# Kernel tuning notes

Hardware: AMD Instinct MI355X
Metric: run time of the kernel (lower is better)

## Reference

```python
import jax, jax.numpy as jnp
import numpy as np

NUM_HEADS = 16
NEG_INF = -1000000.0  # matches torch masked_fill value


def setup_inputs() -> dict:
    key = jax.random.key(0)
    k1, k2, k3, k4, k5, k6 = jax.random.split(key, 6)
    N, S, E = 2, 2048, 1024
    x_encoder = jax.random.normal(k1, (N, S, E), dtype=jnp.float32)
    x_decoder = jax.random.normal(k2, (N, S, E), dtype=jnp.float32)
    mask = jax.random.randint(k3, (S, S), 0, 2, dtype=jnp.int32)
    W_qk = jax.random.normal(k4, (2 * E, E), dtype=jnp.float32) * (1.0 / np.sqrt(E))
    W_v = jax.random.normal(k5, (E, E), dtype=jnp.float32) * (1.0 / np.sqrt(E))
    W_o = jax.random.normal(k6, (E, E), dtype=jnp.float32) * (1.0 / np.sqrt(E))
    return {"x_encoder": x_encoder, "x_decoder": x_decoder, "mask": mask,
            "W_qk": W_qk, "W_v": W_v, "W_o": W_o}


def reference(x_encoder, x_decoder, mask, W_qk, W_v, W_o):
    N, S, E = x_encoder.shape
    H = NUM_HEADS
    hd = E // H
    # projections (no bias)
    qk = x_encoder @ W_qk.T            # (N, S, 2E)
    v = x_decoder @ W_v.T              # (N, S, E)
    qk = qk.reshape(N, S, H, 2 * hd).transpose(0, 2, 1, 3)  # (N, H, S, 2hd)
    v = v.reshape(N, S, H, hd).transpose(0, 2, 1, 3)         # (N, H, S, hd)
    q, k = qk[..., :hd], qk[..., hd:]
    # scaled dot-product attention with mask fill
    logits = jnp.einsum('bhqd,bhkd->bhqk', q, k) / jnp.sqrt(jnp.float32(hd))
    m = mask[None, None, :, :]  # expand_mask: 2D -> (1,1,S,S)
    logits = jnp.where(m == 0, jnp.float32(NEG_INF), logits)
    attn = jax.nn.softmax(logits, axis=-1)
    vals = jnp.einsum('bhqk,bhkd->bhqd', attn, v)            # (N, H, S, hd)
    vals = vals.transpose(0, 2, 1, 3).reshape(N, S, E)
    return vals @ W_o.T
```

## Files before the change

kernel.cpp:

```cpp
#include <hip/hip_runtime.h>

typedef __attribute__((ext_vector_type(8))) short short8;
typedef __attribute__((ext_vector_type(4))) float f32x4;
typedef __attribute__((ext_vector_type(4))) unsigned short u16x4;
typedef __attribute__((ext_vector_type(4))) unsigned int u32x4;

#define MFMA16(A,B,C) __builtin_amdgcn_mfma_f32_16x16x32_bf16(A,B,C,0,0,0)

__device__ __forceinline__ unsigned short f2bf(float f) {
  unsigned int u = __builtin_bit_cast(unsigned int, f);
  unsigned int r = (u + 0x7fffu + ((u >> 16) & 1u)) >> 16;
  return (unsigned short)r;
}

__device__ __forceinline__ unsigned int cvt_pk_bf16(float lo, float hi) {
  unsigned int r;
  asm("v_cvt_pk_bf16_f32 %0, %1, %2" : "=v"(r) : "v"(lo), "v"(hi));
  return r;
}

__device__ __forceinline__ f32x4 zero4() {
  f32x4 z; z.x = 0.f; z.y = 0.f; z.z = 0.f; z.w = 0.f; return z;
}

__device__ __forceinline__ void gl_lds16(const void* g, void* l) {
  __builtin_amdgcn_global_load_lds((const __attribute__((address_space(1))) void*)g,
                                   (__attribute__((address_space(3))) void*)l, 16, 0, 0);
}

__global__ __launch_bounds__(256) void cvt_all(const float* __restrict__ xe,
                                               const float* __restrict__ xd,
                                               const float* __restrict__ wqk,
                                               const float* __restrict__ wv,
                                               const float* __restrict__ wo,
                                               unsigned short* __restrict__ ws) {
  long i = (long)blockIdx.x * 256 + threadIdx.x;
  const float* src; unsigned short* dst; long o; bool scl = false;
  if (i < 1048576)      { src = xe;  dst = ws + 8650752;  o = i; }
  else if (i < 2097152) { src = xd;  dst = ws + 12845056; o = i - 1048576; }
  else if (i < 2621440) { src = wqk; dst = ws + 17039360; o = i - 2097152;
                          scl = (((o >> 8) & 127) < 64); }
  else if (i < 2883584) { src = wv;  dst = ws + 19136512; o = i - 2621440; }
  else                  { src = wo;  dst = ws + 20185088; o = i - 2883584; }
  float4 f = ((const float4*)src)[o];
  if (scl) {
    const float SCQ = 0.125f * 1.4426950408889634f;
    f.x *= SCQ; f.y *= SCQ; f.z *= SCQ; f.w *= SCQ;
  }
  u16x4 r; r.x = f2bf(f.x); r.y = f2bf(f.y); r.z = f2bf(f.z); r.w = f2bf(f.w);
  ((u16x4*)dst)[o] = r;
}

__global__ __launch_bounds__(256) void mask_pack(const int* __restrict__ mask,
                                                 unsigned int* __restrict__ mbits) {
  int idx = blockIdx.x * 256 + threadIdx.x;
  int row = idx >> 6, wi = idx & 63;
  const int* p = mask + (long)row * 2048 + wi * 32;
  unsigned int bits = 0;
  #pragma unroll
  for (int j = 0; j < 32; j++) bits |= (p[j] != 0 ? 1u : 0u) << j;
  mbits[idx] = bits;
}

template <int MODE>
__global__ __launch_bounds__(256) void gemm_bt(const unsigned short* __restrict__ A,
                                               const unsigned short* __restrict__ B,
                                               void* __restrict__ Cv,
                                               int M, int N, int K) {
  __shared__ __align__(16) unsigned short As[128 * 64];
  __shared__ __align__(16) unsigned short Bs[128 * 64];
  const int tid = threadIdx.x;
  const int w = tid >> 6, l = tid & 63;
  const int wr = w >> 1, wc = w & 1;
  const long row0 = (long)blockIdx.y * 128;
  const long col0 = (long)blockIdx.x * 128;
  const int lr = l >> 3;
  const int lc = (l & 7) * 8;

  f32x4 acc[4][4];
  #pragma unroll
  for (int m = 0; m < 4; m++)
    #pragma unroll
    for (int n = 0; n < 4; n++) acc[m][n] = zero4();

  for (int k0 = 0; k0 < K; k0 += 64) {
    #pragma unroll
    for (int j = 0; j < 4; j++) {
      int slot = j * 4 + w;
      int row = slot * 8 + lr;
      gl_lds16(A + (row0 + row) * K + k0 + lc, &As[slot * 512]);
      gl_lds16(B + (col0 + row) * K + k0 + lc, &Bs[slot * 512]);
    }
    __syncthreads();
    #pragma unroll
    for (int kk = 0; kk < 2; kk++) {
      short8 a[4], b[4];
      #pragma unroll
      for (int m = 0; m < 4; m++)
        a[m] = *(const short8*)&As[(wr * 64 + m * 16 + (l & 15)) * 64 + kk * 32 + (l >> 4) * 8];
      #pragma unroll
      for (int n = 0; n < 4; n++)
        b[n] = *(const short8*)&Bs[(wc * 64 + n * 16 + (l & 15)) * 64 + kk * 32 + (l >> 4) * 8];
      #pragma unroll
      for (int m = 0; m < 4; m++)
        #pragma unroll
        for (int n = 0; n < 4; n++)
          acc[m][n] = MFMA16(a[m], b[n], acc[m][n]);
    }
    __syncthreads();
  }

  #pragma unroll
  for (int m = 0; m < 4; m++) {
    long rowb = row0 + wr * 64 + m * 16 + ((l >> 4) * 4);
    #pragma unroll
    for (int n = 0; n < 4; n++) {
      long colb = col0 + wc * 64 + n * 16 + (l & 15);
      if (MODE == 0) {
        unsigned short* C = (unsigned short*)Cv;
        #pragma unroll
        for (int r = 0; r < 4; r++) C[(rowb + r) * N + colb] = f2bf(acc[m][n][r]);
      } else if (MODE == 1) {
        unsigned short* C = (unsigned short*)Cv;
        long bb = rowb >> 11, s0 = rowb & 2047;
        u16x4 pk;
        pk.x = f2bf(acc[m][n][0]); pk.y = f2bf(acc[m][n][1]);
        pk.z = f2bf(acc[m][n][2]); pk.w = f2bf(acc[m][n][3]);
        *(u16x4*)&C[(bb * 1024 + colb) * 2048 + s0] = pk;
      } else {
        float* C = (float*)Cv;
        #pragma unroll
        for (int r = 0; r < 4; r++) C[(rowb + r) * N + colb] = acc[m][n][r];
      }
    }
  }
}

__device__ __forceinline__ void softmax_pack(const f32x4* sf, unsigned long long mw,
                                             int g, int sA, int sB, int gh,
                                             float& l_run, short8& pa0o, short8& pa1o) {
  mw >>= (g * 4);
  unsigned int mlo = (unsigned int)mw, mhi = (unsigned int)(mw >> 32);
  float pv[16];
  float lsum = 0.f;
  #pragma unroll
  for (int kvq = 0; kvq < 4; kvq++) {
    unsigned int msel = (kvq < 2) ? mlo : mhi;
    #pragma unroll
    for (int r = 0; r < 4; r++) {
      float e = __builtin_amdgcn_exp2f(sf[kvq][r]);
      unsigned int bit = (msel >> (((kvq & 1) << 4) + r)) & 1u;
      float p = bit ? e : 0.0f;
      pv[kvq * 4 + r] = p;
      lsum += p;
    }
  }
  l_run += lsum;

  unsigned int pk0[2], pk1[2], pk2[2], pk3[2];
  pk0[0] = cvt_pk_bf16(pv[0],  pv[1]);  pk0[1] = cvt_pk_bf16(pv[2],  pv[3]);
  pk1[0] = cvt_pk_bf16(pv[4],  pv[5]);  pk1[1] = cvt_pk_bf16(pv[6],  pv[7]);
  pk2[0] = cvt_pk_bf16(pv[8],  pv[9]);  pk2[1] = cvt_pk_bf16(pv[10], pv[11]);
  pk3[0] = cvt_pk_bf16(pv[12], pv[13]); pk3[1] = cvt_pk_bf16(pv[14], pv[15]);

  u32x4 a0, a1;
  int t0, t1;
  t0 = __shfl((int)pk0[0], sA); t1 = __shfl((int)pk1[0], sA);
  a0.x = gh ? (unsigned)t1 : (unsigned)t0;
  t0 = __shfl((int)pk0[1], sA); t1 = __shfl((int)pk1[1], sA);
  a0.y = gh ? (unsigned)t1 : (unsigned)t0;
  t0 = __shfl((int)pk0[0], sB); t1 = __shfl((int)pk1[0], sB);
  a0.z = gh ? (unsigned)t1 : (unsigned)t0;
  t0 = __shfl((int)pk0[1], sB); t1 = __shfl((int)pk1[1], sB);
  a0.w = gh ? (unsigned)t1 : (unsigned)t0;
  t0 = __shfl((int)pk2[0], sA); t1 = __shfl((int)pk3[0], sA);
  a1.x = gh ? (unsigned)t1 : (unsigned)t0;
  t0 = __shfl((int)pk2[1], sA); t1 = __shfl((int)pk3[1], sA);
  a1.y = gh ? (unsigned)t1 : (unsigned)t0;
  t0 = __shfl((int)pk2[0], sB); t1 = __shfl((int)pk3[0], sB);
  a1.z = gh ? (unsigned)t1 : (unsigned)t0;
  t0 = __shfl((int)pk2[1], sB); t1 = __shfl((int)pk3[1], sB);
  a1.w = gh ? (unsigned)t1 : (unsigned)t0;
  pa0o = __builtin_bit_cast(short8, a0);
  pa1o = __builtin_bit_cast(short8, a1);
}

__global__ __launch_bounds__(256, 4) void attn(const unsigned short* __restrict__ qk,
                                               const unsigned short* __restrict__ vT,
                                               const unsigned int* __restrict__ mbits,
                                               unsigned short* __restrict__ po0,
                                               unsigned short* __restrict__ po1,
                                               float* __restrict__ pl0,
                                               float* __restrict__ pl1) {
  __shared__ __align__(16) unsigned short Ks[2][64 * 64];
  __shared__ __align__(16) unsigned short Vs[2][64 * 64];
  const int tid = threadIdx.x;
  const int w = tid >> 6, l = tid & 63;
  const int b = blockIdx.z, h = blockIdx.y;
  const int qt = blockIdx.x & 15, kvh = blockIdx.x >> 4;
  const int q0 = qt * 128;
  const int kvbase = kvh << 10;
  unsigned short* po = kvh ? po1 : po0;
  float* pl = kvh ? pl1 : pl0;
  const int c = l & 15, g = l >> 4;
  const int lr = l >> 3, pg = l & 7;

  const int qa = q0 + w * 32 + c;
  const int qb = qa + 16;
  const unsigned short* qptrA = qk + (long)(b * 2048 + qa) * 2048 + h * 128;
  const unsigned short* qptrB = qk + (long)(b * 2048 + qb) * 2048 + h * 128;
  short8 bqA0 = *(const short8*)&qptrA[g * 8];
  short8 bqA1 = *(const short8*)&qptrA[32 + g * 8];
  short8 bqB0 = *(const short8*)&qptrB[g * 8];
  short8 bqB1 = *(const short8*)&qptrB[32 + g * 8];

  const int sw0 = ((g)     ^ (c & 7)) * 8;
  const int sw1 = ((g + 4) ^ (c & 7)) * 8;
  const int sA = c + (((2 * g)     & 3) << 4);
  const int sB = c + (((2 * g + 1) & 3) << 4);
  const int gh = g >> 1;

  const unsigned int* mrowA = mbits + (long)qa * 64;
  const unsigned int* mrowB = mbits + (long)qb * 64;

  const unsigned short* kbase = qk + (long)b * 2048 * 2048 + h * 128 + 64;
  const unsigned short* vbase = vT + (long)((b * 16 + h) * 64) * 2048;
  const int srow = w * 8 + lr;
  const int sgg = pg ^ (lr & 7);

  float lA = 0.f, lB = 0.f;
  f32x4 oA[4], oB[4];
  #pragma unroll
  for (int d = 0; d < 4; d++) { oA[d] = zero4(); oB[d] = zero4(); }

  #pragma unroll
  for (int j = 0; j < 2; j++) {
    int row = srow + j * 32;
    gl_lds16(kbase + (long)(kvbase + row) * 2048 + sgg * 8, &Ks[0][(w + j * 4) * 512]);
    gl_lds16(vbase + (long)row * 2048 + kvbase + sgg * 8,   &Vs[0][(w + j * 4) * 512]);
  }
  __syncthreads();

  for (int it = 0; it < 16; it++) {
    const int kv0 = kvbase + it * 64;
    const int cur = it & 1;

    if (it < 15) {
      #pragma unroll
      for (int j = 0; j < 2; j++) {
        int row = srow + j * 32;
        gl_lds16(kbase + (long)(kv0 + 64 + row) * 2048 + sgg * 8,
                 &Ks[cur ^ 1][(w + j * 4) * 512]);
        gl_lds16(vbase + (long)row * 2048 + kv0 + 64 + sgg * 8,
                 &Vs[cur ^ 1][(w + j * 4) * 512]);
      }
    }

    unsigned long long mwA = *(const unsigned long long*)&mrowA[kv0 >> 5];
    unsigned long long mwB = *(const unsigned long long*)&mrowB[kv0 >> 5];

    f32x4 sfA[4], sfB[4];
    #pragma unroll
    for (int kvq = 0; kvq < 4; kvq++) {
      int R = kvq * 16 + c;
      short8 ak0 = *(const short8*)&Ks[cur][R * 64 + sw0];
      short8 ak1 = *(const short8*)&Ks[cur][R * 64 + sw1];
      f32x4 zA = zero4();
      zA = MFMA16(ak0, bqA0, zA);
      zA = MFMA16(ak1, bqA1, zA);
      sfA[kvq] = zA;
      f32x4 zB = zero4();
      zB = MFMA16(ak0, bqB0, zB);
      zB = MFMA16(ak1, bqB1, zB);
      sfB[kvq] = zB;
    }

    short8 paA0, paA1, paB0, paB1;
    softmax_pack(sfA, mwA, g, sA, sB, gh, lA, paA0, paA1);
    softmax_pack(sfB, mwB, g, sA, sB, gh, lB, paB0, paB1);

    #pragma unroll
    for (int dt = 0; dt < 4; dt++) {
      int d = dt * 16 + c;
      short8 bv0 = *(const short8*)&Vs[cur][d * 64 + sw0];
      short8 bv1 = *(const short8*)&Vs[cur][d * 64 + sw1];
      oA[dt] = MFMA16(paA0, bv0, oA[dt]);
      oA[dt] = MFMA16(paA1, bv1, oA[dt]);
      oB[dt] = MFMA16(paB0, bv0, oB[dt]);
      oB[dt] = MFMA16(paB1, bv1, oB[dt]);
    }

    __syncthreads();
  }

  lA += __shfl_xor(lA, 16); lA += __shfl_xor(lA, 32);
  lB += __shfl_xor(lB, 16); lB += __shfl_xor(lB, 32);
  if (g == 0) {
    pl[((long)(b << 11) + qa) * 16 + h] = lA;
    pl[((long)(b << 11) + qb) * 16 + h] = lB;
  }
  #pragma unroll
  for (int dt = 0; dt < 4; dt++) {
    long rowA = (long)b * 2048 + q0 + w * 32 + g * 4;
    long rowB = rowA + 16;
    int col = h * 64 + dt * 16 + c;
    po[(rowA + 0) * 1024 + col] = f2bf(oA[dt][0]);
    po[(rowA + 1) * 1024 + col] = f2bf(oA[dt][1]);
    po[(rowA + 2) * 1024 + col] = f2bf(oA[dt][2]);
    po[(rowA + 3) * 1024 + col] = f2bf(oA[dt][3]);
    po[(rowB + 0) * 1024 + col] = f2bf(oB[dt][0]);
    po[(rowB + 1) * 1024 + col] = f2bf(oB[dt][1]);
    po[(rowB + 2) * 1024 + col] = f2bf(oB[dt][2]);
    po[(rowB + 3) * 1024 + col] = f2bf(oB[dt][3]);
  }
}

__global__ __launch_bounds__(256) void combine(const unsigned short* __restrict__ po0,
                                               const unsigned short* __restrict__ po1,
                                               const float* __restrict__ pl0,
                                               const float* __restrict__ pl1,
                                               unsigned short* __restrict__ vals) {
  int i = blockIdx.x * 256 + threadIdx.x;
  int q = i >> 7;
  int col = (i & 127) * 8;
  int h = col >> 6;
  float linv = 1.0f / (pl0[q * 16 + h] + pl1[q * 16 + h]);
  long off = (long)q * 1024 + col;
  short8 a = *(const short8*)&po0[off];
  short8 b = *(const short8*)&po1[off];
  short8 o;
  #pragma unroll
  for (int j = 0; j < 8; j++) {
    float fa = __builtin_bit_cast(float, ((unsigned int)(unsigned short)a[j]) << 16);
    float fb = __builtin_bit_cast(float, ((unsigned int)(unsigned short)b[j]) << 16);
    o[j] = (short)f2bf((fa + fb) * linv);
  }
  *(short8*)&vals[off] = o;
}

extern "C" void kernel_launch(void* const* d_in, const int* in_sizes, int n_in,
                              void* d_out, int out_size, void* d_ws, size_t ws_size,
                              hipStream_t stream) {
  const float* xe  = (const float*)d_in[0];
  const float* xd  = (const float*)d_in[1];
  const int*   msk = (const int*)d_in[2];
  const float* wqk = (const float*)d_in[3];
  const float* wv  = (const float*)d_in[4];
  const float* wo  = (const float*)d_in[5];
  float* out = (float*)d_out;
  unsigned short* ws = (unsigned short*)d_ws;

  unsigned short* po0    = ws;
  unsigned short* po1    = ws + 4194304;
  float*          pl0    = (float*)(ws + 8388608);
  float*          pl1    = (float*)(ws + 8519680);
  unsigned short* xe_bf  = ws + 8650752;
  unsigned short* xd_bf  = ws + 12845056;
  unsigned short* wqk_bf = ws + 17039360;
  unsigned short* wv_bf  = ws + 19136512;
  unsigned short* wo_bf  = ws + 20185088;
  unsigned short* qkb    = ws + 21233664;
  unsigned short* vTb    = ws + 29622272;
  unsigned short* valb   = ws + 33816576;
  unsigned int*   mbits  = (unsigned int*)(ws + 38010880);

  cvt_all<<<12288, 256, 0, stream>>>(xe, xd, wqk, wv, wo, ws);
  mask_pack<<<512, 256, 0, stream>>>(msk, mbits);
  gemm_bt<0><<<dim3(16, 32), 256, 0, stream>>>(xe_bf, wqk_bf, qkb, 4096, 2048, 1024);
  gemm_bt<1><<<dim3(8, 32), 256, 0, stream>>>(xd_bf, wv_bf, vTb, 4096, 1024, 1024);
  attn<<<dim3(32, 16, 2), 256, 0, stream>>>(qkb, vTb, mbits, po0, po1, pl0, pl1);
  combine<<<2048, 256, 0, stream>>>(po0, po1, pl0, pl1, valb);
  gemm_bt<2><<<dim3(8, 32), 256, 0, stream>>>(valb, wo_bf, out, 4096, 1024, 1024);
}
```

Measured before the change: 167.6 us.

## Split attention KV into four chunks and merge prep and QKV GEMM launches

The attention kernel now splits the KV range into four 512-key chunks instead of two, doubling the grid to 2048 blocks, and the combine kernel sums four partial outputs and partial row sums. The freed bf16 input buffers are reused as scratch for the extra partials. Mask packing is folded into the conversion kernel, and the QK and V projection GEMMs are merged into one launch. The aim is better GPU occupancy in attention and fewer kernel launches, at the cost of more partial-output traffic and a heavier combine step.

```diff
diff --git a/kernel.cpp b/kernel.cpp
--- a/kernel.cpp
+++ b/kernel.cpp
@@ -28,12 +28,24 @@
                                    (__attribute__((address_space(3))) void*)l, 16, 0, 0);
 }
 
-__global__ __launch_bounds__(256) void cvt_all(const float* __restrict__ xe,
-                                               const float* __restrict__ xd,
-                                               const float* __restrict__ wqk,
-                                               const float* __restrict__ wv,
-                                               const float* __restrict__ wo,
-                                               unsigned short* __restrict__ ws) {
+__global__ __launch_bounds__(256) void prep(const float* __restrict__ xe,
+                                            const float* __restrict__ xd,
+                                            const float* __restrict__ wqk,
+                                            const float* __restrict__ wv,
+                                            const float* __restrict__ wo,
+                                            const int* __restrict__ mask,
+                                            unsigned int* __restrict__ mbits,
+                                            unsigned short* __restrict__ ws) {
+  if (blockIdx.x >= 12288) {
+    int idx = (blockIdx.x - 12288) * 256 + threadIdx.x;
+    int row = idx >> 6, wi = idx & 63;
+    const int* p = mask + (long)row * 2048 + wi * 32;
+    unsigned int bits = 0;
+    #pragma unroll
+    for (int j = 0; j < 32; j++) bits |= (p[j] != 0 ? 1u : 0u) << j;
+    mbits[idx] = bits;
+    return;
+  }
   long i = (long)blockIdx.x * 256 + threadIdx.x;
   const float* src; unsigned short* dst; long o; bool scl = false;
   if (i < 1048576)      { src = xe;  dst = ws + 8650752;  o = i; }
@@ -51,22 +63,82 @@
   ((u16x4*)dst)[o] = r;
 }
 
-__global__ __launch_bounds__(256) void mask_pack(const int* __restrict__ mask,
-                                                 unsigned int* __restrict__ mbits) {
-  int idx = blockIdx.x * 256 + threadIdx.x;
-  int row = idx >> 6, wi = idx & 63;
-  const int* p = mask + (long)row * 2048 + wi * 32;
-  unsigned int bits = 0;
-  #pragma unroll
-  for (int j = 0; j < 32; j++) bits |= (p[j] != 0 ? 1u : 0u) << j;
-  mbits[idx] = bits;
-}
-
-template <int MODE>
-__global__ __launch_bounds__(256) void gemm_bt(const unsigned short* __restrict__ A,
-                                               const unsigned short* __restrict__ B,
-                                               void* __restrict__ Cv,
-                                               int M, int N, int K) {
+__global__ __launch_bounds__(256) void gemm_qkv(const unsigned short* __restrict__ xe,
+                                                const unsigned short* __restrict__ xd,
+                                                const unsigned short* __restrict__ wqk,
+                                                const unsigned short* __restrict__ wv,
+                                                unsigned short* __restrict__ qkb,
+                                                unsigned short* __restrict__ vTb) {
+  __shared__ __align__(16) unsigned short As[128 * 64];
+  __shared__ __align__(16) unsigned short Bs[128 * 64];
+  const int bid = blockIdx.x;
+  const unsigned short* A; const unsigned short* B;
+  long row0, col0; int mode;
+  if (bid < 512) { A = xe; B = wqk; row0 = (long)(bid >> 4) * 128; col0 = (long)(bid & 15) * 128; mode = 0; }
+  else { int id = bid - 512; A = xd; B = wv; row0 = (long)(id >> 3) * 128; col0 = (long)(id & 7) * 128; mode = 1; }
+
+  const int tid = threadIdx.x;
+  const int w = tid >> 6, l = tid & 63;
+  const int wr = w >> 1, wc = w & 1;
+  const int lr = l >> 3;
+  const int lc = (l & 7) * 8;
+
+  f32x4 acc[4][4];
+  #pragma unroll
+  for (int m = 0; m < 4; m++)
+    #pragma unroll
+    for (int n = 0; n < 4; n++) acc[m][n] = zero4();
+
+  for (int k0 = 0; k0 < 1024; k0 += 64) {
+    #pragma unroll
+    for (int j = 0; j < 4; j++) {
+      int slot = j * 4 + w;
+      int row = slot * 8 + lr;
+      gl_lds16(A + (row0 + row) * 1024 + k0 + lc, &As[slot * 512]);
+      gl_lds16(B + (col0 + row) * 1024 + k0 + lc, &Bs[slot * 512]);
+    }
+    __syncthreads();
+    #pragma unroll
+    for (int kk = 0; kk < 2; kk++) {
+      short8 a[4], b[4];
+      #pragma unroll
+      for (int m = 0; m < 4; m++)
+        a[m] = *(const short8*)&As[(wr * 64 + m * 16 + (l & 15)) * 64 + kk * 32 + (l >> 4) * 8];
+      #pragma unroll
+      for (int n = 0; n < 4; n++)
+        b[n] = *(const short8*)&Bs[(wc * 64 + n * 16 + (l & 15)) * 64 + kk * 32 + (l >> 4) * 8];
+      #pragma unroll
+      for (int m = 0; m < 4; m++)
+        #pragma unroll
+        for (int n = 0; n < 4; n++)
+          acc[m][n] = MFMA16(a[m], b[n], acc[m][n]);
+    }
+    __syncthreads();
+  }
+
+  #pragma unroll
+  for (int m = 0; m < 4; m++) {
+    long rowb = row0 + wr * 64 + m * 16 + ((l >> 4) * 4);
+    #pragma unroll
+    for (int n = 0; n < 4; n++) {
+      long colb = col0 + wc * 64 + n * 16 + (l & 15);
+      if (mode == 0) {
+        #pragma unroll
+        for (int r = 0; r < 4; r++) qkb[(rowb + r) * 2048 + colb] = f2bf(acc[m][n][r]);
+      } else {
+        long bb = rowb >> 11, s0 = rowb & 2047;
+        u16x4 pk;
+        pk.x = f2bf(acc[m][n][0]); pk.y = f2bf(acc[m][n][1]);
+        pk.z = f2bf(acc[m][n][2]); pk.w = f2bf(acc[m][n][3]);
+        *(u16x4*)&vTb[(bb * 1024 + colb) * 2048 + s0] = pk;
+      }
+    }
+  }
+}
+
+__global__ __launch_bounds__(256) void gemm_out(const unsigned short* __restrict__ A,
+                                                const unsigned short* __restrict__ B,
+                                                float* __restrict__ C) {
   __shared__ __align__(16) unsigned short As[128 * 64];
   __shared__ __align__(16) unsigned short Bs[128 * 64];
   const int tid = threadIdx.x;
@@ -83,13 +155,13 @@
     #pragma unroll
     for (int n = 0; n < 4; n++) acc[m][n] = zero4();
 
-  for (int k0 = 0; k0 < K; k0 += 64) {
+  for (int k0 = 0; k0 < 1024; k0 += 64) {
     #pragma unroll
     for (int j = 0; j < 4; j++) {
       int slot = j * 4 + w;
       int row = slot * 8 + lr;
-      gl_lds16(A + (row0 + row) * K + k0 + lc, &As[slot * 512]);
-      gl_lds16(B + (col0 + row) * K + k0 + lc, &Bs[slot * 512]);
+      gl_lds16(A + (row0 + row) * 1024 + k0 + lc, &As[slot * 512]);
+      gl_lds16(B + (col0 + row) * 1024 + k0 + lc, &Bs[slot * 512]);
     }
     __syncthreads();
     #pragma unroll
@@ -116,22 +188,8 @@
     #pragma unroll
     for (int n = 0; n < 4; n++) {
       long colb = col0 + wc * 64 + n * 16 + (l & 15);
-      if (MODE == 0) {
-        unsigned short* C = (unsigned short*)Cv;
-        #pragma unroll
-        for (int r = 0; r < 4; r++) C[(rowb + r) * N + colb] = f2bf(acc[m][n][r]);
-      } else if (MODE == 1) {
-        unsigned short* C = (unsigned short*)Cv;
-        long bb = rowb >> 11, s0 = rowb & 2047;
-        u16x4 pk;
-        pk.x = f2bf(acc[m][n][0]); pk.y = f2bf(acc[m][n][1]);
-        pk.z = f2bf(acc[m][n][2]); pk.w = f2bf(acc[m][n][3]);
-        *(u16x4*)&C[(bb * 1024 + colb) * 2048 + s0] = pk;
-      } else {
-        float* C = (float*)Cv;
-        #pragma unroll
-        for (int r = 0; r < 4; r++) C[(rowb + r) * N + colb] = acc[m][n][r];
-      }
+      #pragma unroll
+      for (int r = 0; r < 4; r++) C[(rowb + r) * 1024 + colb] = acc[m][n][r];
     }
   }
 }
@@ -190,8 +248,12 @@
                                                const unsigned int* __restrict__ mbits,
                                                unsigned short* __restrict__ po0,
                                                unsigned short* __restrict__ po1,
+                                               unsigned short* __restrict__ po2,
+                                               unsigned short* __restrict__ po3,
                                                float* __restrict__ pl0,
-                                               float* __restrict__ pl1) {
+                                               float* __restrict__ pl1,
+                                               float* __restrict__ pl2,
+                                               float* __restrict__ pl3) {
   __shared__ __align__(16) unsigned short Ks[2][64 * 64];
   __shared__ __align__(16) unsigned short Vs[2][64 * 64];
   const int tid = threadIdx.x;
@@ -199,9 +261,9 @@
   const int b = blockIdx.z, h = blockIdx.y;
   const int qt = blockIdx.x & 15, kvh = blockIdx.x >> 4;
   const int q0 = qt * 128;
-  const int kvbase = kvh << 10;
-  unsigned short* po = kvh ? po1 : po0;
-  float* pl = kvh ? pl1 : pl0;
+  const int kvbase = kvh << 9;
+  unsigned short* po = (kvh == 0) ? po0 : (kvh == 1) ? po1 : (kvh == 2) ? po2 : po3;
+  float* pl = (kvh == 0) ? pl0 : (kvh == 1) ? pl1 : (kvh == 2) ? pl2 : pl3;
   const int c = l & 15, g = l >> 4;
   const int lr = l >> 3, pg = l & 7;
 
@@ -241,11 +303,11 @@
   }
   __syncthreads();
 
-  for (int it = 0; it < 16; it++) {
+  for (int it = 0; it < 8; it++) {
     const int kv0 = kvbase + it * 64;
     const int cur = it & 1;
 
-    if (it < 15) {
+    if (it < 7) {
       #pragma unroll
       for (int j = 0; j < 2; j++) {
         int row = srow + j * 32;
@@ -317,23 +379,31 @@
 
 __global__ __launch_bounds__(256) void combine(const unsigned short* __restrict__ po0,
                                                const unsigned short* __restrict__ po1,
+                                               const unsigned short* __restrict__ po2,
+                                               const unsigned short* __restrict__ po3,
                                                const float* __restrict__ pl0,
                                                const float* __restrict__ pl1,
+                                               const float* __restrict__ pl2,
+                                               const float* __restrict__ pl3,
                                                unsigned short* __restrict__ vals) {
   int i = blockIdx.x * 256 + threadIdx.x;
   int q = i >> 7;
   int col = (i & 127) * 8;
   int h = col >> 6;
-  float linv = 1.0f / (pl0[q * 16 + h] + pl1[q * 16 + h]);
+  float linv = 1.0f / (pl0[q * 16 + h] + pl1[q * 16 + h] + pl2[q * 16 + h] + pl3[q * 16 + h]);
   long off = (long)q * 1024 + col;
   short8 a = *(const short8*)&po0[off];
   short8 b = *(const short8*)&po1[off];
+  short8 cc = *(const short8*)&po2[off];
+  short8 d = *(const short8*)&po3[off];
   short8 o;
   #pragma unroll
   for (int j = 0; j < 8; j++) {
     float fa = __builtin_bit_cast(float, ((unsigned int)(unsigned short)a[j]) << 16);
     float fb = __builtin_bit_cast(float, ((unsigned int)(unsigned short)b[j]) << 16);
-    o[j] = (short)f2bf((fa + fb) * linv);
+    float fc = __builtin_bit_cast(float, ((unsigned int)(unsigned short)cc[j]) << 16);
+    float fd = __builtin_bit_cast(float, ((unsigned int)(unsigned short)d[j]) << 16);
+    o[j] = (short)f2bf((fa + fb + fc + fd) * linv);
   }
   *(short8*)&vals[off] = o;
 }
@@ -363,12 +433,15 @@
   unsigned short* vTb    = ws + 29622272;
   unsigned short* valb   = ws + 33816576;
   unsigned int*   mbits  = (unsigned int*)(ws + 38010880);
-
-  cvt_all<<<12288, 256, 0, stream>>>(xe, xd, wqk, wv, wo, ws);
-  mask_pack<<<512, 256, 0, stream>>>(msk, mbits);
-  gemm_bt<0><<<dim3(16, 32), 256, 0, stream>>>(xe_bf, wqk_bf, qkb, 4096, 2048, 1024);
-  gemm_bt<1><<<dim3(8, 32), 256, 0, stream>>>(xd_bf, wv_bf, vTb, 4096, 1024, 1024);
-  attn<<<dim3(32, 16, 2), 256, 0, stream>>>(qkb, vTb, mbits, po0, po1, pl0, pl1);
-  combine<<<2048, 256, 0, stream>>>(po0, po1, pl0, pl1, valb);
-  gemm_bt<2><<<dim3(8, 32), 256, 0, stream>>>(valb, wo_bf, out, 4096, 1024, 1024);
-}
+  unsigned short* po2    = xe_bf;
+  unsigned short* po3    = xd_bf;
+  float*          pl2    = (float*)wqk_bf;
+  float*          pl3    = (float*)(wqk_bf + 131072);
+
+  prep<<<12800, 256, 0, stream>>>(xe, xd, wqk, wv, wo, msk, mbits, ws);
+  gemm_qkv<<<768, 256, 0, stream>>>(xe_bf, xd_bf, wqk_bf, wv_bf, qkb, vTb);
+  attn<<<dim3(64, 16, 2), 256, 0, stream>>>(qkb, vTb, mbits,
+                                            po0, po1, po2, po3, pl0, pl1, pl2, pl3);
+  combine<<<2048, 256, 0, stream>>>(po0, po1, po2, po3, pl0, pl1, pl2, pl3, valb);
+  gemm_out<<<dim3(8, 32), 256, 0, stream>>>(valb, wo_bf, out);
+}
```

Result: no change. 170.0 us (+1.5%).
